# Kernel tuning notes

Measured on AMD Instinct MI355X. Metric: run time of the kernel, lower is better.

## Reference

```python
import jax, jax.numpy as jnp
import numpy as np

B, C, L = 8, 256, 2048        # batch, query_dim, seq len
HEADS, DIM_HEAD = 4, 32
HIDDEN = HEADS * DIM_HEAD      # 128
EPS = 1e-05
SCALE = DIM_HEAD ** -0.5


def setup_inputs() -> dict:
    key = jax.random.key(0)
    ks = jax.random.split(key, 8)
    s_in = 1.0 / np.sqrt(C)
    s_h = 1.0 / np.sqrt(HIDDEN)
    return {
        "x": jax.random.normal(ks[0], (B, C, L), dtype=jnp.float32),
        "g": jnp.ones((1, C, 1), dtype=jnp.float32),
        "b": jnp.zeros((1, C, 1), dtype=jnp.float32),
        "Wq": jax.random.normal(ks[1], (HIDDEN, C), dtype=jnp.float32) * s_in,
        "Wk": jax.random.normal(ks[2], (HIDDEN, C), dtype=jnp.float32) * s_in,
        "Wv": jax.random.normal(ks[3], (HIDDEN, C), dtype=jnp.float32) * s_in,
        "Wo": jax.random.normal(ks[4], (C, HIDDEN), dtype=jnp.float32) * s_h,
        "bo": jnp.zeros((C,), dtype=jnp.float32),
    }


def reference(x, g, b, Wq, Wk, Wv, Wo, bo):
    og_x = x
    # channel-dim LayerNorm (dim=1), biased variance
    mean = jnp.mean(x, axis=1, keepdims=True)
    var = jnp.var(x, axis=1, keepdims=True)
    xn = (x - mean) / jnp.sqrt(var + EPS) * g + b          # [B, C, L]
    xt = jnp.transpose(xn, (0, 2, 1))                      # [B, L, C]
    # QKV projections (self-attention: context = normed x)
    q = xt @ Wq.T                                          # [B, L, HIDDEN]
    k = xt @ Wk.T
    v = xt @ Wv.T
    # b (h c) d layout: [B, HEADS, DIM_HEAD, L]
    split = lambda t: jnp.transpose(t, (0, 2, 1)).reshape(B, HEADS, DIM_HEAD, L)
    q, k, v = split(q), split(k), split(v)
    # scores over head-channel dim c -> [B, H, L, L]
    qk = jnp.einsum('bhcd,bhce->bhde', q, k) * SCALE
    attn = jax.nn.softmax(qk, axis=-1)
    out = jnp.einsum('bhde,bhce->bhcd', attn, v)           # [B, H, DIM_HEAD, L]
    out = out.reshape(B, HIDDEN, L)
    # 1x1 Conv1d: hidden -> query_dim
    y = jnp.einsum('oc,bcl->bol', Wo, out) + bo[None, :, None]
    return y + og_x
```

## Files before the change

### kernel.cpp

```cpp
#include <hip/hip_runtime.h>
#include <math.h>

#define BB_ 8
#define CC_ 256
#define LL_ 2048
#define HEADS_ 4
#define DHEAD_ 32
#define HID_ 128
#define EPS_ 1e-5f
#define SCALE_ 0.17677669529663687f
#define K1_ (SCALE_ * 1.44269504088896f)

typedef short v8s  __attribute__((ext_vector_type(8)));
typedef float v4f  __attribute__((ext_vector_type(4)));
typedef float v16f __attribute__((ext_vector_type(16)));
typedef unsigned v4u __attribute__((ext_vector_type(4)));

__device__ inline short f2bf(float x) {
    union { float f; unsigned u; } a; a.f = x;
    unsigned r = a.u + 0x7fffu + ((a.u >> 16) & 1u);
    return (short)(r >> 16);
}
__device__ inline unsigned fbits(float x) { union { float f; unsigned u; } a; a.f = x; return a.u; }

__global__ __launch_bounds__(256) void k_prep(
    const float* __restrict__ Wq, const float* __restrict__ Wk, const float* __restrict__ Wv,
    const float* __restrict__ Wo, const float* __restrict__ g, const float* __restrict__ bvec,
    short* __restrict__ wqkv, short* __restrict__ wo, float2* __restrict__ gb)
{
    __shared__ float red0[4], red1[4];
    const int blk = blockIdx.x, c = threadIdx.x;
    const int wave = c >> 6, lane = c & 63;
    if (blk < 384) {
        const float* W; int oo; float scale = 1.f;
        if (blk < 128)      { W = Wq; oo = blk;       scale = K1_; }
        else if (blk < 256) { W = Wk; oo = blk - 128; }
        else                { W = Wv; oo = blk - 256; }
        float w  = W[oo * 256 + c] * scale;
        float wg = w * g[c];
        wqkv[blk * 256 + c] = f2bf(wg);
        float r0 = wg, r1 = w * bvec[c];
        #pragma unroll
        for (int off = 1; off < 64; off <<= 1) {
            r0 += __shfl_xor(r0, off, 64);
            r1 += __shfl_xor(r1, off, 64);
        }
        if (lane == 0) { red0[wave] = r0; red1[wave] = r1; }
        __syncthreads();
        if (c == 0)
            gb[blk] = make_float2(red0[0] + red0[1] + red0[2] + red0[3],
                                  red1[0] + red1[1] + red1[2] + red1[3]);
    } else {
        int i2 = (blk - 384) * 256 + c;
        wo[i2] = f2bf(Wo[i2]);
    }
}

__global__ __launch_bounds__(512) void k_ln_qkv(
    const float* __restrict__ x, const short* __restrict__ wqkv, const float2* __restrict__ gb,
    short* __restrict__ q, short* __restrict__ k, short* __restrict__ v)
{
    __shared__ short xnT[32 * 264];
    __shared__ short st2[128 * 48];
    __shared__ float ps_[8 * 32], ps2_[8 * 32];
    const int b   = blockIdx.y;
    const int l0  = blockIdx.x * 32;
    const int tid = threadIdx.x;
    const int wave = tid >> 6, lane = tid & 63;

    {
        const int ls = tid & 31;
        const int cg = tid >> 5;
        float s = 0.f, s2 = 0.f;
        #pragma unroll
        for (int kk = 0; kk < 8; ++kk) {
            int c = 2 * cg + 32 * kk;
            float t0 = x[((size_t)b * CC_ + c) * LL_ + l0 + ls];
            float t1 = x[((size_t)b * CC_ + c + 1) * LL_ + l0 + ls];
            s += t0 + t1; s2 += t0 * t0 + t1 * t1;
            unsigned pk = (unsigned short)f2bf(t0) | ((unsigned)(unsigned short)f2bf(t1) << 16);
            *(unsigned*)(xnT + ls * 264 + c) = pk;
        }
        s  += __shfl_xor(s, 32, 64);
        s2 += __shfl_xor(s2, 32, 64);
        if (lane < 32) { ps_[wave * 32 + lane] = s; ps2_[wave * 32 + lane] = s2; }
    }
    __syncthreads();

    const int n = lane & 15, quad = lane >> 4;
    const int rowbase = (wave >> 2) * 16;
    const int colbase = (wave & 3) * 96;

    v4f acc[6];
    #pragma unroll
    for (int ct = 0; ct < 6; ++ct) acc[ct] = (v4f){0.f, 0.f, 0.f, 0.f};

    #pragma unroll
    for (int ks = 0; ks < 8; ++ks) {
        const v8s af = *(const v8s*)(xnT + (rowbase + n) * 264 + ks * 32 + quad * 8);
        #pragma unroll
        for (int ct = 0; ct < 6; ++ct) {
            const v8s bfrag = *(const v8s*)(wqkv + (size_t)(colbase + ct * 16 + n) * 256 + ks * 32 + quad * 8);
            acc[ct] = __builtin_amdgcn_mfma_f32_16x16x32_bf16(af, bfrag, acc[ct], 0, 0, 0);
        }
    }
    __syncthreads();

    float rsv[4], rmv[4];
    #pragma unroll
    for (int r = 0; r < 4; ++r) {
        int l = rowbase + quad * 4 + r;
        float s = 0.f, s2 = 0.f;
        #pragma unroll
        for (int p = 0; p < 8; ++p) { s += ps_[p * 32 + l]; s2 += ps2_[p * 32 + l]; }
        float mean = s * (1.f / CC_);
        float var  = s2 * (1.f / CC_) - mean * mean;
        float rs   = rsqrtf(var + EPS_);
        rsv[r] = rs; rmv[r] = rs * mean;
    }
    #pragma unroll
    for (int ct = 0; ct < 6; ++ct) {
        int o = colbase + ct * 16 + n;
        float2 gbo = gb[o];
        #pragma unroll
        for (int r = 0; r < 4; ++r) {
            int l = rowbase + quad * 4 + r;
            float val = rsv[r] * acc[ct][r] - rmv[r] * gbo.x + gbo.y;
            if (o < 256)      xnT[l * 264 + o] = f2bf(val);
            else              st2[(o - 256) * 48 + l] = f2bf(val);
        }
    }
    __syncthreads();

    {
        int u = tid;
        int h = u >> 7, rest = u & 127;
        int l = rest >> 2, dg = rest & 3;
        size_t bh = (size_t)b * HEADS_ + h;
        v8s qv = *(const v8s*)(xnT + l * 264 + h * 32 + dg * 8);
        *(v8s*)(q + (bh * LL_ + l0 + l) * DHEAD_ + dg * 8) = qv;
        v8s kv = *(const v8s*)(xnT + l * 264 + 128 + h * 32 + dg * 8);
        *(v8s*)(k + (bh * LL_ + l0 + l) * DHEAD_ + dg * 8) = kv;

        int op = u >> 2, lg = u & 3;
        v8s vv = *(const v8s*)(st2 + op * 48 + lg * 8);
        int h2 = op >> 5, d = op & 31;
        *(v8s*)(v + (((size_t)b * HEADS_ + h2) * DHEAD_ + d) * LL_ + l0 + lg * 8) = vv;
    }
}

#define CHK_ 256
__global__ __launch_bounds__(256) void k_attn(
    const short* __restrict__ q, const short* __restrict__ k, const short* __restrict__ v,
    short* __restrict__ ao)
{
    __shared__ short Kb[CHK_ * 40];
    __shared__ short Vb[32 * 264];
    const int bh   = blockIdx.y;
    const int b    = bh >> 2, h = bh & 3;
    const int tid  = threadIdx.x;
    const int wave = tid >> 6, lane = tid & 63;
    const int m    = lane & 31;
    const int half = lane >> 5;
    const size_t kvbase = (size_t)bh * LL_ * DHEAD_;
    const size_t vbase  = (size_t)bh * DHEAD_ * LL_;

    const int q0 = blockIdx.x * 128 + wave * 32;

    const v8s qf0 = *(const v8s*)(q + kvbase + (size_t)(q0 + m) * DHEAD_ + half * 8);
    const v8s qf1 = *(const v8s*)(q + kvbase + (size_t)(q0 + m) * DHEAD_ + 16 + half * 8);

    v16f O = {};
    float psum = 0.f;

    for (int kc = 0; kc < LL_; kc += CHK_) {
        __syncthreads();
        {
            const short* src = k + kvbase + (size_t)(kc + tid) * DHEAD_;
            short* dst = Kb + tid * 40;
            #pragma unroll
            for (int j = 0; j < 4; ++j)
                *(v8s*)(dst + j * 8) = *(const v8s*)(src + j * 8);
        }
        {
            const int col = (tid & 31) * 8, dr = tid >> 5;
            #pragma unroll
            for (int p = 0; p < 4; ++p) {
                int d = p * 8 + dr;
                *(v8s*)(Vb + d * 264 + col) =
                    *(const v8s*)(v + vbase + (size_t)d * LL_ + kc + col);
            }
        }
        __syncthreads();

        #pragma unroll
        for (int ktl = 0; ktl < CHK_; ktl += 32) {
            const v8s kf0 = *(const v8s*)(Kb + (ktl + m) * 40 + half * 8);
            const v8s kf1 = *(const v8s*)(Kb + (ktl + m) * 40 + 16 + half * 8);
            v16f S = __builtin_amdgcn_mfma_f32_32x32x16_bf16(kf0, qf0, (v16f){}, 0, 0, 0);
            S      = __builtin_amdgcn_mfma_f32_32x32x16_bf16(kf1, qf1, S,        0, 0, 0);

            const v8s vf0 = *(const v8s*)(Vb + m * 264 + ktl + half * 8);
            const v8s vf1 = *(const v8s*)(Vb + m * 264 + ktl + 16 + half * 8);

            unsigned e[8];
            #pragma unroll
            for (int i = 0; i < 8; ++i) {
                float pa = __builtin_amdgcn_exp2f(S[2 * i]);
                float pb = __builtin_amdgcn_exp2f(S[2 * i + 1]);
                psum += pa + pb;
                e[i] = __builtin_amdgcn_perm(fbits(pb) + 0x8000u, fbits(pa) + 0x8000u, 0x07060302u);
            }
            v4u f1, f2;
#if __has_builtin(__builtin_amdgcn_permlane32_swap)
            {
                auto r02 = __builtin_amdgcn_permlane32_swap(e[0], e[2], false, false);
                auto r13 = __builtin_amdgcn_permlane32_swap(e[1], e[3], false, false);
                auto r46 = __builtin_amdgcn_permlane32_swap(e[4], e[6], false, false);
                auto r57 = __builtin_amdgcn_permlane32_swap(e[5], e[7], false, false);
                f1 = (v4u){r02[0], r13[0], r02[1], r13[1]};
                f2 = (v4u){r46[0], r57[0], r46[1], r57[1]};
            }
#else
            {
                unsigned o0 = __shfl_xor(e[0], 32, 64), o1 = __shfl_xor(e[1], 32, 64);
                unsigned o2 = __shfl_xor(e[2], 32, 64), o3 = __shfl_xor(e[3], 32, 64);
                unsigned o4 = __shfl_xor(e[4], 32, 64), o5 = __shfl_xor(e[5], 32, 64);
                unsigned o6 = __shfl_xor(e[6], 32, 64), o7 = __shfl_xor(e[7], 32, 64);
                f1 = half ? (v4u){o2, o3, e[2], e[3]} : (v4u){e[0], e[1], o0, o1};
                f2 = half ? (v4u){o6, o7, e[6], e[7]} : (v4u){e[4], e[5], o4, o5};
            }
#endif
            O = __builtin_amdgcn_mfma_f32_32x32x16_bf16(__builtin_bit_cast(v8s, f1), vf0, O, 0, 0, 0);
            O = __builtin_amdgcn_mfma_f32_32x32x16_bf16(__builtin_bit_cast(v8s, f2), vf1, O, 0, 0, 0);
        }
    }

    psum += __shfl_xor(psum, 32, 64);
    float invden = 1.f / psum;
    #pragma unroll
    for (int r = 0; r < 16; ++r) {
        int qr = (r & 3) + 8 * (r >> 2) + 4 * half;
        float inv = __shfl(invden, qr, 64);
        int row = q0 + qr;
        ao[((size_t)b * LL_ + row) * HID_ + h * DHEAD_ + m] = f2bf(O[r] * inv);
    }
}

__global__ __launch_bounds__(256) void k_oproj(
    const short* __restrict__ ao, const short* __restrict__ wo, const float* __restrict__ bo,
    const float* __restrict__ x, float* __restrict__ out)
{
    const int b = blockIdx.z;
    const int l0 = blockIdx.x * 32;
    const int tid = threadIdx.x;
    const int wave = tid >> 6, lane = tid & 63;
    const int m = lane & 31, half = lane >> 5;
    const int o0 = blockIdx.y * 128 + wave * 32;

    v8s bf[8];
    #pragma unroll
    for (int ks = 0; ks < 8; ++ks)
        bf[ks] = *(const v8s*)(ao + ((size_t)b * LL_ + l0 + m) * HID_ + ks * 16 + half * 8);

    v16f acc = {};
    #pragma unroll
    for (int ks = 0; ks < 8; ++ks) {
        const v8s af = *(const v8s*)(wo + (size_t)(o0 + m) * HID_ + ks * 16 + half * 8);
        acc = __builtin_amdgcn_mfma_f32_32x32x16_bf16(af, bf[ks], acc, 0, 0, 0);
    }

    #pragma unroll
    for (int r = 0; r < 16; ++r) {
        int o = o0 + (r & 3) + 8 * (r >> 2) + 4 * half;
        size_t oi = ((size_t)b * CC_ + o) * LL_ + l0 + m;
        out[oi] = acc[r] + bo[o] + x[oi];
    }
}

extern "C" void kernel_launch(void* const* d_in, const int* in_sizes, int n_in,
                              void* d_out, int out_size, void* d_ws, size_t ws_size,
                              hipStream_t stream) {
    const float* x  = (const float*)d_in[0];
    const float* g  = (const float*)d_in[1];
    const float* bv = (const float*)d_in[2];
    const float* Wq = (const float*)d_in[3];
    const float* Wk = (const float*)d_in[4];
    const float* Wv = (const float*)d_in[5];
    const float* Wo = (const float*)d_in[6];
    const float* bo = (const float*)d_in[7];
    float* out = (float*)d_out;

    const size_t qkv_elems = (size_t)BB_ * HEADS_ * LL_ * DHEAD_;
    short* q    = (short*)d_ws;
    short* k    = q + qkv_elems;
    short* v    = k + qkv_elems;
    short* ao   = v + qkv_elems;
    short* wqkv = ao + qkv_elems;
    short* wo   = wqkv + 384 * 256;
    float2* gb  = (float2*)(wo + 256 * 128);

    k_prep  <<<dim3(512), dim3(256), 0, stream>>>(Wq, Wk, Wv, Wo, g, bv, wqkv, wo, gb);
    k_ln_qkv<<<dim3(LL_ / 32, BB_), dim3(512), 0, stream>>>(x, wqkv, gb, q, k, v);
    k_attn  <<<dim3(LL_ / 128, BB_ * HEADS_), dim3(256), 0, stream>>>(q, k, v, ao);
    k_oproj <<<dim3(LL_ / 32, 2, BB_), dim3(256), 0, stream>>>(ao, wo, bo, x, out);
}
```

Baseline: 163.2 us.

## Split attention key range across two wave groups and merge partials in LDS

The attention kernel now runs 512 threads per block. Two groups of four waves each process one half of the key sequence for the same 128 queries, and their partial outputs and row sums are combined through shared memory at the end. The goal is more waves per block to hide MFMA, exp and LDS latency, with the same 512 blocks in the grid. The cost is an extra reduction pass with two barriers, more shared memory per block, and idle waves during the final write.

```diff
diff --git a/kernel.cpp b/kernel.cpp
--- a/kernel.cpp
+++ b/kernel.cpp
@@ -149,23 +149,28 @@
     }
 }
 
-#define CHK_ 256
-__global__ __launch_bounds__(256) void k_attn(
+__global__ __launch_bounds__(512) void k_attn(
     const short* __restrict__ q, const short* __restrict__ k, const short* __restrict__ v,
     short* __restrict__ ao)
 {
-    __shared__ short Kb[CHK_ * 40];
-    __shared__ short Vb[32 * 264];
+    __shared__ char smem[20480 + 17408 + 512];
+    short* Kb     = (short*)smem;
+    short* Vb     = (short*)(smem + 20480);
+    float* Ost    = (float*)smem;
+    float* psumst = (float*)(smem + 20480 + 17408);
+
     const int bh   = blockIdx.y;
     const int b    = bh >> 2, h = bh & 3;
     const int tid  = threadIdx.x;
     const int wave = tid >> 6, lane = tid & 63;
+    const int wq   = wave & 3;
+    const int kh   = wave >> 2;
     const int m    = lane & 31;
     const int half = lane >> 5;
     const size_t kvbase = (size_t)bh * LL_ * DHEAD_;
     const size_t vbase  = (size_t)bh * DHEAD_ * LL_;
 
-    const int q0 = blockIdx.x * 128 + wave * 32;
+    const int q0 = blockIdx.x * 128 + wq * 32;
 
     const v8s qf0 = *(const v8s*)(q + kvbase + (size_t)(q0 + m) * DHEAD_ + half * 8);
     const v8s qf1 = *(const v8s*)(q + kvbase + (size_t)(q0 + m) * DHEAD_ + 16 + half * 8);
@@ -173,35 +178,40 @@
     v16f O = {};
     float psum = 0.f;
 
-    for (int kc = 0; kc < LL_; kc += CHK_) {
+    const int s_hh  = (tid >> 7) & 1;
+    const int s_r   = tid & 127;
+    const int s_p   = tid >> 8;
+    const int v_hh  = tid >> 8;
+    const int v_d   = (tid >> 3) & 31;
+    const int v_cg  = tid & 7;
+
+    for (int kc = 0; kc < 1024; kc += 128) {
         __syncthreads();
         {
-            const short* src = k + kvbase + (size_t)(kc + tid) * DHEAD_;
-            short* dst = Kb + tid * 40;
-            #pragma unroll
-            for (int j = 0; j < 4; ++j)
-                *(v8s*)(dst + j * 8) = *(const v8s*)(src + j * 8);
+            const short* src = k + kvbase + (size_t)(s_hh * 1024 + kc + s_r) * DHEAD_ + s_p * 16;
+            short* dst = Kb + s_hh * 5120 + s_r * 40 + s_p * 16;
+            *(v8s*)dst       = *(const v8s*)src;
+            *(v8s*)(dst + 8) = *(const v8s*)(src + 8);
         }
         {
-            const int col = (tid & 31) * 8, dr = tid >> 5;
-            #pragma unroll
-            for (int p = 0; p < 4; ++p) {
-                int d = p * 8 + dr;
-                *(v8s*)(Vb + d * 264 + col) =
-                    *(const v8s*)(v + vbase + (size_t)d * LL_ + kc + col);
-            }
+            const short* src = v + vbase + (size_t)v_d * LL_ + v_hh * 1024 + kc + v_cg * 16;
+            short* dst = Vb + v_hh * 4352 + v_d * 136 + v_cg * 16;
+            *(v8s*)dst       = *(const v8s*)src;
+            *(v8s*)(dst + 8) = *(const v8s*)(src + 8);
         }
         __syncthreads();
 
-        #pragma unroll
-        for (int ktl = 0; ktl < CHK_; ktl += 32) {
-            const v8s kf0 = *(const v8s*)(Kb + (ktl + m) * 40 + half * 8);
-            const v8s kf1 = *(const v8s*)(Kb + (ktl + m) * 40 + 16 + half * 8);
+        const short* Kw = Kb + kh * 5120;
+        const short* Vw = Vb + kh * 4352;
+        #pragma unroll
+        for (int ktl = 0; ktl < 128; ktl += 32) {
+            const v8s kf0 = *(const v8s*)(Kw + (ktl + m) * 40 + half * 8);
+            const v8s kf1 = *(const v8s*)(Kw + (ktl + m) * 40 + 16 + half * 8);
             v16f S = __builtin_amdgcn_mfma_f32_32x32x16_bf16(kf0, qf0, (v16f){}, 0, 0, 0);
             S      = __builtin_amdgcn_mfma_f32_32x32x16_bf16(kf1, qf1, S,        0, 0, 0);
 
-            const v8s vf0 = *(const v8s*)(Vb + m * 264 + ktl + half * 8);
-            const v8s vf1 = *(const v8s*)(Vb + m * 264 + ktl + 16 + half * 8);
+            const v8s vf0 = *(const v8s*)(Vw + m * 136 + ktl + half * 8);
+            const v8s vf1 = *(const v8s*)(Vw + m * 136 + ktl + 16 + half * 8);
 
             unsigned e[8];
             #pragma unroll
@@ -237,13 +247,28 @@
     }
 
     psum += __shfl_xor(psum, 32, 64);
-    float invden = 1.f / psum;
-    #pragma unroll
-    for (int r = 0; r < 16; ++r) {
-        int qr = (r & 3) + 8 * (r >> 2) + 4 * half;
-        float inv = __shfl(invden, qr, 64);
-        int row = q0 + qr;
-        ao[((size_t)b * LL_ + row) * HID_ + h * DHEAD_ + m] = f2bf(O[r] * inv);
+
+    __syncthreads();
+    if (kh == 1) {
+        #pragma unroll
+        for (int r = 0; r < 16; ++r) {
+            int qr = (r & 3) + 8 * (r >> 2) + 4 * half;
+            Ost[(wq * 32 + qr) * 32 + m] = O[r];
+        }
+        if (half == 0) psumst[wq * 32 + m] = psum;
+    }
+    __syncthreads();
+    if (kh == 0) {
+        float den = psum + psumst[wq * 32 + m];
+        float invden = 1.f / den;
+        #pragma unroll
+        for (int r = 0; r < 16; ++r) {
+            int qr = (r & 3) + 8 * (r >> 2) + 4 * half;
+            float inv = __shfl(invden, qr, 64);
+            float val = (O[r] + Ost[(wq * 32 + qr) * 32 + m]) * inv;
+            int row = q0 + qr;
+            ao[((size_t)b * LL_ + row) * HID_ + h * DHEAD_ + m] = f2bf(val);
+        }
     }
 }
 
@@ -302,6 +327,6 @@
 
     k_prep  <<<dim3(512), dim3(256), 0, stream>>>(Wq, Wk, Wv, Wo, g, bv, wqkv, wo, gb);
     k_ln_qkv<<<dim3(LL_ / 32, BB_), dim3(512), 0, stream>>>(x, wqkv, gb, q, k, v);
-    k_attn  <<<dim3(LL_ / 128, BB_ * HEADS_), dim3(256), 0, stream>>>(q, k, v, ao);
+    k_attn  <<<dim3(LL_ / 128, BB_ * HEADS_), dim3(512), 0, stream>>>(q, k, v, ao);
     k_oproj <<<dim3(LL_ / 32, 2, BB_), dim3(256), 0, stream>>>(ao, wo, bo, x, out);
 }
```

Result: faster. 157.3 us (-3.7%).
